# Performance work log

Measured on AMD Instinct MI355X. Metric: run time of the kernel, lower is better.

Reference implementation:

```python
import jax, jax.numpy as jnp
import numpy as np

CLS_NUM, INPUT_DIM, BATCH = 1024, 512, 16384
TAU = 0.1       # gumbel-softmax temperature from F.gumbel_softmax(sim, tau=0.1)
EPS = 1e-12     # F.normalize eps


def _l2norm(x):
    # F.normalize(x, p=2, dim=1)
    n = jnp.sqrt(jnp.sum(x * x, axis=1, keepdims=True))
    return x / jnp.maximum(n, EPS)


def setup_inputs() -> dict:
    key = jax.random.key(0)
    k1, k2, k3 = jax.random.split(key, 3)
    # xavier_uniform bound for [cls_num, input_dim]
    bound = float(np.sqrt(6.0 / (CLS_NUM + INPUT_DIM)))
    return {
        "input": jax.random.normal(k1, (BATCH, INPUT_DIM), dtype=jnp.float32),
        "prototypes_para": jax.random.uniform(k2, (CLS_NUM, INPUT_DIM), dtype=jnp.float32, minval=-bound, maxval=bound),
        "gumbel_u": jax.random.uniform(k3, (BATCH, CLS_NUM), dtype=jnp.float32, minval=1e-6, maxval=1.0 - 1e-6),
    }


def reference(input, prototypes_para, gumbel_u):
    x = _l2norm(input)                 # [B, D]
    p = _l2norm(prototypes_para)       # [K, D]
    # Original: broadcast x and p to [B, K, D] (via multiply-by-ones) then cosine.
    # Since both are unit-norm, cosine similarity == dot product -> one matmul.
    # Input is .detach()'d in the original, so stop_gradient on x here.
    sim = jax.lax.stop_gradient(x) @ p.T                    # [B, K]
    # Gumbel-softmax (soft): softmax((logits + gumbel)/tau)
    g = -jnp.log(-jnp.log(gumbel_u))
    e = jax.nn.softmax((sim + g) / TAU, axis=-1)            # [B, K]
    pt = jnp.einsum('bk,kv->bv', e, p)                      # [B, D]
    sim_loss = jnp.mean(1.0 - jnp.einsum('bk,bk->b', e, sim))
    # Nested i!=j pairwise cosine loop == sum of P P^T minus its diagonal
    ppt = p @ p.T                                           # [K, K]
    div_loss = jnp.sum(ppt) - jnp.sum(jnp.diagonal(ppt))
    return pt, p, sim_loss, div_loss
```

## Files before the change

### kernel.cpp

```cpp
#include <hip/hip_runtime.h>
#include <math.h>

#define B  16384
#define K  1024
#define D  512
#define EPS 1e-12f

#define SM_C1 14.426950408889634f
#define SM_C2 5.287663729448977f

typedef unsigned short ushort_t;

#define LOG2F(x) __builtin_amdgcn_logf(x)
#define EXP2F(x) __builtin_amdgcn_exp2f(x)

#define OUT_PT   0
#define OUT_P    (B*D)
#define OUT_SIM  (B*D + K*D)
#define OUT_DIV  (B*D + K*D + 1)

#define WS_RED   1024
#define WS_SIM   32768
#define WS_PH    (WS_SIM + (B*K)/2)
#define WS_PTH   (WS_PH + (K*D)/2)
#define WS_DIAGP (WS_PTH + (K*D)/2)
#define WS_COLP  (WS_DIAGP + 256)


typedef _Float16 half8 __attribute__((ext_vector_type(8)));
typedef float f32x4 __attribute__((ext_vector_type(4)));

__device__ __forceinline__ float wave_reduce_sum(float v) {
    #pragma unroll
    for (int off = 32; off >= 1; off >>= 1) v += __shfl_down(v, off);
    return v;
}
__device__ __forceinline__ float wave_reduce_max(float v) {
    #pragma unroll
    for (int off = 32; off >= 1; off >>= 1) v = fmaxf(v, __shfl_down(v, off));
    return v;
}

__device__ __forceinline__ ushort_t f2h(float f) {
    _Float16 h = (_Float16)f;
    return __builtin_bit_cast(ushort_t, h);
}
__device__ __forceinline__ float h2f(ushort_t u) {
    return (float)__builtin_bit_cast(_Float16, u);
}

__device__ __forceinline__ void async16(const void* g, void* l) {
    __builtin_amdgcn_global_load_lds(
        (const __attribute__((address_space(1))) unsigned int*)g,
        (__attribute__((address_space(3))) unsigned int*)l, 16, 0, 0);
}

__global__ __launch_bounds__(256) void prep_kernel(const float* __restrict__ proto,
                                                   const float* __restrict__ x,
                                                   float* __restrict__ out,
                                                   float* __restrict__ ws,
                                                   ushort_t* __restrict__ Ph,
                                                   ushort_t* __restrict__ Xh) {
    __shared__ float cs[4][512];
    __shared__ float red[4];
    int tid = threadIdx.x, wid = tid >> 6, lane = tid & 63;

    if (blockIdx.x < 256) {
        int row = blockIdx.x * 4 + wid;
        const float4* pr = (const float4*)(proto + (size_t)row * D);
        float4 a = pr[lane * 2], b = pr[lane * 2 + 1];
        float ss = a.x*a.x + a.y*a.y + a.z*a.z + a.w*a.w
                 + b.x*b.x + b.y*b.y + b.z*b.z + b.w*b.w;
        ss = wave_reduce_sum(ss);
        ss = __shfl(ss, 0);
        float inv = 1.0f / fmaxf(sqrtf(ss), EPS);
        float4 na = make_float4(a.x*inv, a.y*inv, a.z*inv, a.w*inv);
        float4 nb = make_float4(b.x*inv, b.y*inv, b.z*inv, b.w*inv);
        float4* po = (float4*)(out + OUT_P + (size_t)row * D);
        po[lane * 2]     = na;
        po[lane * 2 + 1] = nb;
        ushort4* ph = (ushort4*)(Ph + (size_t)row * D);
        ph[lane * 2]     = make_ushort4(f2h(na.x), f2h(na.y), f2h(na.z), f2h(na.w));
        ph[lane * 2 + 1] = make_ushort4(f2h(nb.x), f2h(nb.y), f2h(nb.z), f2h(nb.w));
        *(float4*)(&cs[wid][lane * 8])     = na;
        *(float4*)(&cs[wid][lane * 8 + 4]) = nb;
        if (lane == 0) red[wid] = ss * inv * inv;
        __syncthreads();
        float c0 = cs[0][tid] + cs[1][tid] + cs[2][tid] + cs[3][tid];
        float c1 = cs[0][tid + 256] + cs[1][tid + 256] + cs[2][tid + 256] + cs[3][tid + 256];
        ws[WS_COLP + (size_t)blockIdx.x * 512 + tid]       = c0;
        ws[WS_COLP + (size_t)blockIdx.x * 512 + tid + 256] = c1;
        if (tid == 0) ws[WS_DIAGP + blockIdx.x] = red[0] + red[1] + red[2] + red[3];
    } else {
        int row = (blockIdx.x - 256) * 4 + wid;
        const float4* xr = (const float4*)(x + (size_t)row * D);
        float4 a = xr[lane * 2], b = xr[lane * 2 + 1];
        float ss = a.x*a.x + a.y*a.y + a.z*a.z + a.w*a.w
                 + b.x*b.x + b.y*b.y + b.z*b.z + b.w*b.w;
        ss = wave_reduce_sum(ss);
        ss = __shfl(ss, 0);
        float inv = 1.0f / fmaxf(sqrtf(ss), EPS);
        ushort4 h0 = make_ushort4(f2h(a.x*inv), f2h(a.y*inv), f2h(a.z*inv), f2h(a.w*inv));
        ushort4 h1 = make_ushort4(f2h(b.x*inv), f2h(b.y*inv), f2h(b.z*inv), f2h(b.w*inv));
        ushort4* xo = (ushort4*)(Xh + (size_t)row * D);
        xo[lane * 2]     = h0;
        xo[lane * 2 + 1] = h1;
    }
}

template<int LDA, int LDB, int LDC, int KK, bool F16C, int NBN, int NBM, int EXTRA>
__global__ __launch_bounds__(256) void gemm_bt2(const ushort_t* __restrict__ A,
                                                const ushort_t* __restrict__ Bm,
                                                void* __restrict__ Cv,
                                                const float* __restrict__ phat,
                                                ushort_t* __restrict__ PT,
                                                float* __restrict__ out,
                                                float* __restrict__ ws) {
    __shared__ __align__(16) char smem[64 * 65 * 4];
    int tid = threadIdx.x;
    int wid = tid >> 6, lane = tid & 63;

    if (blockIdx.x >= NBM * NBN) {
        if (EXTRA == 1) {
            int pid = blockIdx.x - NBM * NBN;
            int k0 = (pid & 15) * 64, d0 = (pid >> 4) * 64;
            float (*tile)[65] = (float(*)[65])smem;
            #pragma unroll
            for (int i = tid; i < 64 * 64; i += 256) {
                int kk = i >> 6, dd = i & 63;
                tile[dd][kk] = phat[(size_t)(k0 + kk) * D + d0 + dd];
            }
            __syncthreads();
            #pragma unroll
            for (int i = tid; i < 64 * 64; i += 256) {
                int dd = i >> 6, kk = i & 63;
                PT[(size_t)(d0 + dd) * K + k0 + kk] = f2h(tile[dd][kk]);
            }
        } else if (EXTRA == 2) {
            float* rd = (float*)smem;
            float* rs = rd + 4;
            float* rg = rs + 4;
            float vdot = 0.0f;
            #pragma unroll
            for (int i = 0; i < 4; ++i) vdot += ws[WS_RED + tid + 256 * i];
            float diag = ws[WS_DIAGP + tid];
            float c0 = 0.0f, c1 = 0.0f;
            #pragma unroll 8
            for (int b2 = 0; b2 < 256; ++b2) {
                c0 += ws[WS_COLP + (size_t)b2 * 512 + tid];
                c1 += ws[WS_COLP + (size_t)b2 * 512 + tid + 256];
            }
            float vssq = c0 * c0 + c1 * c1;
            vdot = wave_reduce_sum(vdot);
            vssq = wave_reduce_sum(vssq);
            diag = wave_reduce_sum(diag);
            if (lane == 0) { rd[wid] = vdot; rs[wid] = vssq; rg[wid] = diag; }
            __syncthreads();
            if (tid == 0) {
                float dot = rd[0] + rd[1] + rd[2] + rd[3];
                float ssq = rs[0] + rs[1] + rs[2] + rs[3];
                float dg  = rg[0] + rg[1] + rg[2] + rg[3];
                out[OUT_SIM] = 1.0f - dot * (1.0f / (float)B);
                out[OUT_DIV] = ssq - dg;
            }
        }
        return;
    }

    ushort_t* As = (ushort_t*)smem;
    ushort_t* Bs = (ushort_t*)(smem + 8192);

    int quad = lane >> 4, l16 = lane & 15;
    int wm = (wid & 1) * 64, wn = (wid >> 1) * 64;

    int sid = blockIdx.x;
    int xcd = sid & 7, slot = sid >> 3;
    int bmb = xcd * (NBM / 8) + slot / NBN;
    int bnb = slot % NBN;
    int bn0 = bnb * 128, bm0 = bmb * 128;

    int ldrow = lane >> 2;
    int lcol  = (lane & 3) * 8;

    f32x4 acc[4][4] = {};

    ushort_t* AsD[2][2] = {
        { As + (wid * 16) * 32,        As + (64 + wid * 16) * 32 },
        { As + 4096 + (wid * 16) * 32, As + 4096 + (64 + wid * 16) * 32 } };
    ushort_t* BsD[2][2] = {
        { Bs + (wid * 16) * 32,        Bs + (64 + wid * 16) * 32 },
        { Bs + 4096 + (wid * 16) * 32, Bs + 4096 + (64 + wid * 16) * 32 } };

    const ushort_t* Ab = A + (size_t)(bm0 + wid * 16 + ldrow) * LDA + lcol;
    const ushort_t* Bb = Bm + (size_t)(bn0 + wid * 16 + ldrow) * LDB + lcol;

    for (int kc = 0; kc < KK; kc += 64) {
        async16(Ab + kc,                       AsD[0][0]);
        async16(Ab + kc + (size_t)64 * LDA,    AsD[0][1]);
        async16(Ab + kc + 32,                  AsD[1][0]);
        async16(Ab + kc + 32 + (size_t)64*LDA, AsD[1][1]);
        async16(Bb + kc,                       BsD[0][0]);
        async16(Bb + kc + (size_t)64 * LDB,    BsD[0][1]);
        async16(Bb + kc + 32,                  BsD[1][0]);
        async16(Bb + kc + 32 + (size_t)64*LDB, BsD[1][1]);
        __syncthreads();
        #pragma unroll
        for (int p = 0; p < 2; ++p) {
            half8 af[4], bg[4];
            #pragma unroll
            for (int i = 0; i < 4; ++i)
                af[i] = *(const half8*)(As + p * 4096 + (wm + 16 * i + l16) * 32 + quad * 8);
            #pragma unroll
            for (int j = 0; j < 4; ++j)
                bg[j] = *(const half8*)(Bs + p * 4096 + (wn + 16 * j + l16) * 32 + quad * 8);
            #pragma unroll
            for (int i = 0; i < 4; ++i)
                #pragma unroll
                for (int j = 0; j < 4; ++j)
                    acc[i][j] = __builtin_amdgcn_mfma_f32_16x16x32_f16(af[i], bg[j], acc[i][j], 0, 0, 0);
        }
        __syncthreads();
    }
    #pragma unroll
    for (int i = 0; i < 4; ++i) {
        #pragma unroll
        for (int j = 0; j < 4; ++j) {
            #pragma unroll
            for (int r = 0; r < 4; ++r) {
                int row = bm0 + wm + 16 * i + quad * 4 + r;
                int col = bn0 + wn + 16 * j + l16;
                if (F16C)
                    ((ushort_t*)Cv)[(size_t)row * LDC + col] = f2h(acc[i][j][r]);
                else
                    ((float*)Cv)[(size_t)row * LDC + col] = acc[i][j][r];
            }
        }
    }
}

__global__ __launch_bounds__(256) void softmax_rows(const float* __restrict__ u,
                                                    float* __restrict__ ws) {
    ushort_t* simh = (ushort_t*)(ws + WS_SIM);
    int tid = threadIdx.x;
    int wid = tid >> 6, lane = tid & 63;
    int gw = blockIdx.x * 4 + wid;
    float dotacc = 0.0f;

    for (int r = 0; r < 4; ++r) {
        int row = gw + 4096 * r;
        ushort4* srow = (ushort4*)(simh + (size_t)row * K);
        const float4* urow = (const float4*)(u + (size_t)row * K);
        float4 s[4], z[4];
        #pragma unroll
        for (int j = 0; j < 4; ++j) {
            ushort4 sh = srow[lane + 64 * j];
            float4 uu = urow[lane + 64 * j];
            s[j] = make_float4(h2f(sh.x), h2f(sh.y), h2f(sh.z), h2f(sh.w));
            z[j].x = SM_C1 * s[j].x - 10.0f * LOG2F(-LOG2F(uu.x)) + SM_C2;
            z[j].y = SM_C1 * s[j].y - 10.0f * LOG2F(-LOG2F(uu.y)) + SM_C2;
            z[j].z = SM_C1 * s[j].z - 10.0f * LOG2F(-LOG2F(uu.z)) + SM_C2;
            z[j].w = SM_C1 * s[j].w - 10.0f * LOG2F(-LOG2F(uu.w)) + SM_C2;
        }
        float m = z[0].x;
        #pragma unroll
        for (int j = 0; j < 4; ++j)
            m = fmaxf(m, fmaxf(fmaxf(z[j].x, z[j].y), fmaxf(z[j].z, z[j].w)));
        m = wave_reduce_max(m);
        m = __shfl(m, 0);

        float4 e[4];
        float l = 0.0f;
        #pragma unroll
        for (int j = 0; j < 4; ++j) {
            e[j].x = EXP2F(z[j].x - m);
            e[j].y = EXP2F(z[j].y - m);
            e[j].z = EXP2F(z[j].z - m);
            e[j].w = EXP2F(z[j].w - m);
            l += e[j].x + e[j].y + e[j].z + e[j].w;
        }
        l = wave_reduce_sum(l);
        l = __shfl(l, 0);
        float inv = 1.0f / l;

        #pragma unroll
        for (int j = 0; j < 4; ++j) {
            float ex = e[j].x * inv, ey = e[j].y * inv,
                  ez = e[j].z * inv, ew = e[j].w * inv;
            srow[lane + 64 * j] = make_ushort4(f2h(ex), f2h(ey), f2h(ez), f2h(ew));
            dotacc += ex * s[j].x + ey * s[j].y + ez * s[j].z + ew * s[j].w;
        }
    }

    dotacc = wave_reduce_sum(dotacc);
    __shared__ float red[4];
    if (lane == 0) red[wid] = dotacc;
    __syncthreads();
    if (tid == 0) ws[WS_RED + blockIdx.x] = red[0] + red[1] + red[2] + red[3];
}

extern "C" void kernel_launch(void* const* d_in, const int* in_sizes, int n_in,
                              void* d_out, int out_size, void* d_ws, size_t ws_size,
                              hipStream_t stream) {
    const float* input  = (const float*)d_in[0];
    const float* proto  = (const float*)d_in[1];
    const float* gumbel = (const float*)d_in[2];
    float* out = (float*)d_out;
    float* ws  = (float*)d_ws;

    ushort_t* Xh   = (ushort_t*)(out + OUT_PT);
    ushort_t* Ph   = (ushort_t*)(ws + WS_PH);
    ushort_t* PTh  = (ushort_t*)(ws + WS_PTH);
    ushort_t* simh = (ushort_t*)(ws + WS_SIM);

    prep_kernel<<<256 + B / 4, 256, 0, stream>>>(proto, input, out, ws, Ph, Xh);

    gemm_bt2<512, 512, K, 512, true, 8, 128, 1>
        <<<(K / 128) * (B / 128) + 128, 256, 0, stream>>>(
            Xh, Ph, simh, out + OUT_P, PTh, out, ws);

    softmax_rows<<<1024, 256, 0, stream>>>(gumbel, ws);

    gemm_bt2<1024, 1024, D, 1024, false, 4, 128, 2>
        <<<(D / 128) * (B / 128) + 1, 256, 0, stream>>>(
            simh, PTh, out + OUT_PT, out + OUT_P, PTh, out, ws);
}
```

Measured before the change: 191.2 us.

## Double-buffer GEMM k-loop with async prefetch and raise MFMA priority

The GEMM main loop now uses a 32-wide k step with two shared-memory buffers. The next tile is prefetched asynchronously while MFMAs run on the current one, synchronised with explicit vmcnt waits and raw s_barrier, and wave priority is raised around the MFMA block. This aims to hide global-to-LDS latency that the old load-then-sync-then-compute loop exposed. The final loss reduction also moves to double precision for accuracy, which adds a small cost in a single block. Risks are more barriers per k step because the chunks are smaller, and correctness depends on the hand-set vmcnt count matching the number of async loads.

```diff
diff --git a/kernel.cpp b/kernel.cpp
--- a/kernel.cpp
+++ b/kernel.cpp
@@ -31,6 +31,11 @@
 typedef float f32x4 __attribute__((ext_vector_type(4)));
 
 __device__ __forceinline__ float wave_reduce_sum(float v) {
+    #pragma unroll
+    for (int off = 32; off >= 1; off >>= 1) v += __shfl_down(v, off);
+    return v;
+}
+__device__ __forceinline__ double wave_reduce_sum_d(double v) {
     #pragma unroll
     for (int off = 32; off >= 1; off >>= 1) v += __shfl_down(v, off);
     return v;
@@ -109,14 +114,14 @@
 }
 
 template<int LDA, int LDB, int LDC, int KK, bool F16C, int NBN, int NBM, int EXTRA>
-__global__ __launch_bounds__(256) void gemm_bt2(const ushort_t* __restrict__ A,
+__global__ __launch_bounds__(256) void gemm_bt3(const ushort_t* __restrict__ A,
                                                 const ushort_t* __restrict__ Bm,
                                                 void* __restrict__ Cv,
                                                 const float* __restrict__ phat,
                                                 ushort_t* __restrict__ PT,
                                                 float* __restrict__ out,
                                                 float* __restrict__ ws) {
-    __shared__ __align__(16) char smem[64 * 65 * 4];
+    __shared__ __align__(16) char smem[32768];
     int tid = threadIdx.x;
     int wid = tid >> 6, lane = tid & 63;
 
@@ -137,38 +142,37 @@
                 PT[(size_t)(d0 + dd) * K + k0 + kk] = f2h(tile[dd][kk]);
             }
         } else if (EXTRA == 2) {
-            float* rd = (float*)smem;
-            float* rs = rd + 4;
-            float* rg = rs + 4;
-            float vdot = 0.0f;
-            #pragma unroll
-            for (int i = 0; i < 4; ++i) vdot += ws[WS_RED + tid + 256 * i];
-            float diag = ws[WS_DIAGP + tid];
-            float c0 = 0.0f, c1 = 0.0f;
-            #pragma unroll 8
+            double* rd = (double*)smem;
+            double* rs = rd + 4;
+            double* rg = rs + 4;
+            double vdot = 0.0;
+            #pragma unroll
+            for (int i = 0; i < 4; ++i) vdot += (double)ws[WS_RED + tid + 256 * i];
+            double diag = (double)ws[WS_DIAGP + tid];
+            double c0 = 0.0, c1 = 0.0;
             for (int b2 = 0; b2 < 256; ++b2) {
-                c0 += ws[WS_COLP + (size_t)b2 * 512 + tid];
-                c1 += ws[WS_COLP + (size_t)b2 * 512 + tid + 256];
-            }
-            float vssq = c0 * c0 + c1 * c1;
-            vdot = wave_reduce_sum(vdot);
-            vssq = wave_reduce_sum(vssq);
-            diag = wave_reduce_sum(diag);
+                c0 += (double)ws[WS_COLP + (size_t)b2 * 512 + tid];
+                c1 += (double)ws[WS_COLP + (size_t)b2 * 512 + tid + 256];
+            }
+            double vssq = c0 * c0 + c1 * c1;
+            vdot = wave_reduce_sum_d(vdot);
+            vssq = wave_reduce_sum_d(vssq);
+            diag = wave_reduce_sum_d(diag);
             if (lane == 0) { rd[wid] = vdot; rs[wid] = vssq; rg[wid] = diag; }
             __syncthreads();
             if (tid == 0) {
-                float dot = rd[0] + rd[1] + rd[2] + rd[3];
-                float ssq = rs[0] + rs[1] + rs[2] + rs[3];
-                float dg  = rg[0] + rg[1] + rg[2] + rg[3];
-                out[OUT_SIM] = 1.0f - dot * (1.0f / (float)B);
-                out[OUT_DIV] = ssq - dg;
+                double dot = rd[0] + rd[1] + rd[2] + rd[3];
+                double ssq = rs[0] + rs[1] + rs[2] + rs[3];
+                double dg  = rg[0] + rg[1] + rg[2] + rg[3];
+                out[OUT_SIM] = (float)(1.0 - dot * (1.0 / (double)B));
+                out[OUT_DIV] = (float)(ssq - dg);
             }
         }
         return;
     }
 
     ushort_t* As = (ushort_t*)smem;
-    ushort_t* Bs = (ushort_t*)(smem + 8192);
+    ushort_t* Bs = (ushort_t*)(smem + 16384);
 
     int quad = lane >> 4, l16 = lane & 15;
     int wm = (wid & 1) * 64, wn = (wid >> 1) * 64;
@@ -184,43 +188,47 @@
 
     f32x4 acc[4][4] = {};
 
-    ushort_t* AsD[2][2] = {
-        { As + (wid * 16) * 32,        As + (64 + wid * 16) * 32 },
-        { As + 4096 + (wid * 16) * 32, As + 4096 + (64 + wid * 16) * 32 } };
-    ushort_t* BsD[2][2] = {
-        { Bs + (wid * 16) * 32,        Bs + (64 + wid * 16) * 32 },
-        { Bs + 4096 + (wid * 16) * 32, Bs + 4096 + (64 + wid * 16) * 32 } };
-
     const ushort_t* Ab = A + (size_t)(bm0 + wid * 16 + ldrow) * LDA + lcol;
     const ushort_t* Bb = Bm + (size_t)(bn0 + wid * 16 + ldrow) * LDB + lcol;
 
-    for (int kc = 0; kc < KK; kc += 64) {
-        async16(Ab + kc,                       AsD[0][0]);
-        async16(Ab + kc + (size_t)64 * LDA,    AsD[0][1]);
-        async16(Ab + kc + 32,                  AsD[1][0]);
-        async16(Ab + kc + 32 + (size_t)64*LDA, AsD[1][1]);
-        async16(Bb + kc,                       BsD[0][0]);
-        async16(Bb + kc + (size_t)64 * LDB,    BsD[0][1]);
-        async16(Bb + kc + 32,                  BsD[1][0]);
-        async16(Bb + kc + 32 + (size_t)64*LDB, BsD[1][1]);
-        __syncthreads();
-        #pragma unroll
-        for (int p = 0; p < 2; ++p) {
+    auto stage = [&](int buf, int kc) {
+        async16(Ab + kc,                    As + buf * 4096 + (wid * 16) * 32);
+        async16(Ab + kc + (size_t)64 * LDA, As + buf * 4096 + (64 + wid * 16) * 32);
+        async16(Bb + kc,                    Bs + buf * 4096 + (wid * 16) * 32);
+        async16(Bb + kc + (size_t)64 * LDB, Bs + buf * 4096 + (64 + wid * 16) * 32);
+    };
+
+    constexpr int NT = KK / 32;
+    stage(0, 0);
+    for (int t = 0; t < NT; ++t) {
+        if (t + 1 < NT) {
+            stage((t + 1) & 1, (t + 1) * 32);
+            asm volatile("s_waitcnt vmcnt(4)" ::: "memory");
+        } else {
+            asm volatile("s_waitcnt vmcnt(0)" ::: "memory");
+        }
+        __builtin_amdgcn_s_barrier();
+        __builtin_amdgcn_sched_barrier(0);
+        {
+            int buf = t & 1;
             half8 af[4], bg[4];
             #pragma unroll
             for (int i = 0; i < 4; ++i)
-                af[i] = *(const half8*)(As + p * 4096 + (wm + 16 * i + l16) * 32 + quad * 8);
+                af[i] = *(const half8*)(As + buf * 4096 + (wm + 16 * i + l16) * 32 + quad * 8);
             #pragma unroll
             for (int j = 0; j < 4; ++j)
-                bg[j] = *(const half8*)(Bs + p * 4096 + (wn + 16 * j + l16) * 32 + quad * 8);
+                bg[j] = *(const half8*)(Bs + buf * 4096 + (wn + 16 * j + l16) * 32 + quad * 8);
+            __builtin_amdgcn_s_setprio(1);
             #pragma unroll
             for (int i = 0; i < 4; ++i)
                 #pragma unroll
                 for (int j = 0; j < 4; ++j)
                     acc[i][j] = __builtin_amdgcn_mfma_f32_16x16x32_f16(af[i], bg[j], acc[i][j], 0, 0, 0);
-        }
-        __syncthreads();
-    }
+            __builtin_amdgcn_s_setprio(0);
+        }
+        if (t + 1 < NT) __builtin_amdgcn_s_barrier();
+    }
+
     #pragma unroll
     for (int i = 0; i < 4; ++i) {
         #pragma unroll
@@ -314,13 +322,13 @@
 
     prep_kernel<<<256 + B / 4, 256, 0, stream>>>(proto, input, out, ws, Ph, Xh);
 
-    gemm_bt2<512, 512, K, 512, true, 8, 128, 1>
+    gemm_bt3<512, 512, K, 512, true, 8, 128, 1>
         <<<(K / 128) * (B / 128) + 128, 256, 0, stream>>>(
             Xh, Ph, simh, out + OUT_P, PTh, out, ws);
 
     softmax_rows<<<1024, 256, 0, stream>>>(gumbel, ws);
 
-    gemm_bt2<1024, 1024, D, 1024, false, 4, 128, 2>
+    gemm_bt3<1024, 1024, D, 1024, false, 4, 128, 2>
         <<<(D / 128) * (B / 128) + 1, 256, 0, stream>>>(
             simh, PTh, out + OUT_PT, out + OUT_P, PTh, out, ws);
 }
```

Measured after the change: 195.3 us. +2.2%, slower.
